# Kernel optimization log

Measured on AMD Instinct MI355X. Metric: run time of the kernel, lower is better.

## Reference

```python
import jax, jax.numpy as jnp
import numpy as np

N_NODES = 100000
N_EDGES = 800000
IN_DIM = 7
HID = 64
HEADS1 = 4
NUM_CLUSTERS = 4
NEG_SLOPE = 0.2


def setup_inputs() -> dict:
    key = jax.random.key(0)
    ks = jax.random.split(key, 24)
    s = 0.1
    inp = {
        "x": jax.random.uniform(ks[0], (N_NODES, IN_DIM), dtype=jnp.float32),
        "edge_index": jax.random.randint(ks[1], (2, N_EDGES), 0, N_NODES, dtype=jnp.int32),
        "edge_attr": jax.random.normal(ks[2], (N_EDGES, 1), dtype=jnp.float32),
        "assignments": jax.random.randint(ks[3], (N_NODES,), 0, NUM_CLUSTERS, dtype=jnp.int32),
        "W1": jax.random.normal(ks[4], (IN_DIM, HEADS1 * HID), dtype=jnp.float32) * s,
        "att_src1": jax.random.normal(ks[5], (HEADS1, HID), dtype=jnp.float32) * s,
        "att_dst1": jax.random.normal(ks[6], (HEADS1, HID), dtype=jnp.float32) * s,
        "We1": jax.random.normal(ks[7], (1, HEADS1 * HID), dtype=jnp.float32) * s,
        "att_e1": jax.random.normal(ks[8], (HEADS1, HID), dtype=jnp.float32) * s,
        "b1": jnp.zeros((HEADS1 * HID,), dtype=jnp.float32),
        "W2": jax.random.normal(ks[9], (HEADS1 * HID, HID), dtype=jnp.float32) * s,
        "att_src2": jax.random.normal(ks[10], (1, HID), dtype=jnp.float32) * s,
        "att_dst2": jax.random.normal(ks[11], (1, HID), dtype=jnp.float32) * s,
        "We2": jax.random.normal(ks[12], (1, HID), dtype=jnp.float32) * s,
        "att_e2": jax.random.normal(ks[13], (1, HID), dtype=jnp.float32) * s,
        "b2": jnp.zeros((HID,), dtype=jnp.float32),
        # actor MLP: (HID+1) -> HID -> 1
        "A1": jax.random.normal(ks[14], (HID + 1, HID), dtype=jnp.float32) * s,
        "ba1": jnp.zeros((HID,), dtype=jnp.float32),
        "A2": jax.random.normal(ks[15], (HID, 1), dtype=jnp.float32) * s,
        "ba2": jnp.zeros((1,), dtype=jnp.float32),
        # critic MLP: HID*num_clusters -> HID -> 1
        "C1": jax.random.normal(ks[16], (HID * NUM_CLUSTERS, HID), dtype=jnp.float32) * s,
        "bc1": jnp.zeros((HID,), dtype=jnp.float32),
        "C2": jax.random.normal(ks[17], (HID, 1), dtype=jnp.float32) * s,
        "bc2": jnp.zeros((1,), dtype=jnp.float32),
    }
    return inp


def _segment_softmax(logits, seg, n):
    # logits: [E, H]; softmax over edges sharing the same dst node.
    m = jax.ops.segment_max(logits, seg, num_segments=n)
    e = jnp.exp(logits - m[seg])
    z = jax.ops.segment_sum(e, seg, num_segments=n)
    return e / z[seg]


def _gat_conv(x, edge_index, edge_attr, W, att_src, att_dst, We, att_e, bias,
              heads, out_dim, concat, n):
    src, dst = edge_index[0], edge_index[1]
    xh = (x @ W).reshape(n, heads, out_dim)                   # [N,H,D]
    a_src = (xh * att_src[None]).sum(-1)                      # [N,H]
    a_dst = (xh * att_dst[None]).sum(-1)                      # [N,H]
    eh = (edge_attr @ We).reshape(-1, heads, out_dim)         # [E,H,D]
    a_e = (eh * att_e[None]).sum(-1)                          # [E,H]
    alpha = jax.nn.leaky_relu(a_src[src] + a_dst[dst] + a_e, NEG_SLOPE)
    alpha = _segment_softmax(alpha, dst, n)                   # [E,H]
    msg = xh[src] * alpha[:, :, None]                         # [E,H,D]
    out = jax.ops.segment_sum(msg, dst, num_segments=n)       # [N,H,D]
    out = out.reshape(n, heads * out_dim) if concat else out.mean(axis=1)
    return out + bias


def reference(x, edge_index, edge_attr, assignments,
              W1, att_src1, att_dst1, We1, att_e1, b1,
              W2, att_src2, att_dst2, We2, att_e2, b2,
              A1, ba1, A2, ba2, C1, bc1, C2, bc2):
    n = x.shape[0]
    h = jax.nn.elu(_gat_conv(x, edge_index, edge_attr,
                             W1, att_src1, att_dst1, We1, att_e1, b1,
                             HEADS1, HID, True, n))
    h = _gat_conv(h, edge_index, edge_attr,
                  W2, att_src2, att_dst2, We2, att_e2, b2,
                  1, HID, False, n)                            # [N,HID]
    # cluster mean pooling (fused segment-reduce, replaces python loop)
    seg = assignments
    counts = jax.ops.segment_sum(jnp.ones((n,), dtype=h.dtype), seg,
                                 num_segments=NUM_CLUSTERS)
    denom = jnp.maximum(counts, 1.0)[:, None]
    z_clusters = jax.ops.segment_sum(h, seg, num_segments=NUM_CLUSTERS) / denom
    z_clusters = jnp.where(counts[:, None] > 0, z_clusters, 0.0)  # [C,HID]
    cf = jax.ops.segment_sum(x[:, 6], seg, num_segments=NUM_CLUSTERS) / denom[:, 0]
    cf = jnp.where(counts > 0, cf, 0.0)[:, None]                  # [C,1]
    z_with_cf = jnp.concatenate([z_clusters, cf], axis=-1)        # [C,HID+1]
    logits = (jax.nn.relu(z_with_cf @ A1 + ba1) @ A2 + ba2)[:, 0]  # [C]
    z_flat = z_clusters.reshape(1, -1)                             # [1,C*HID]
    value = jax.nn.relu(z_flat @ C1 + bc1) @ C2 + bc2              # [1,1]
    probs = jax.nn.softmax(logits)[None, :]                        # [1,C]
    return probs, value, z_flat
```

## Files before the change

### kernel.cpp

```cpp
#include <hip/hip_runtime.h>
#include <hip/hip_fp16.h>

#define NN 100000
#define NE 800000
#define NZB (NN / 32)
#define SRCMASK 0x01FFFFFF

typedef short bf16x8 __attribute__((ext_vector_type(8)));
typedef float f32x4 __attribute__((ext_vector_type(4)));

__device__ __forceinline__ float wave_reduce_sum(float v) {
    #pragma unroll
    for (int o = 32; o > 0; o >>= 1) v += __shfl_down(v, o, 64);
    return v;
}

__device__ __forceinline__ unsigned short f2bf(float f) {
    unsigned u = __float_as_uint(f);
    unsigned r = (u + 0x7FFFu + ((u >> 16) & 1u)) >> 16;
    return (unsigned short)r;
}
__device__ __forceinline__ float bf2f(unsigned short b) {
    return __uint_as_float(((unsigned)b) << 16);
}
__device__ __forceinline__ float bflo(unsigned u) {
    return __uint_as_float(u << 16);
}
__device__ __forceinline__ float bfhi(unsigned u) {
    return __uint_as_float(u & 0xFFFF0000u);
}
__device__ __forceinline__ unsigned pk2(float a, float b) {
    return (unsigned)f2bf(a) | ((unsigned)f2bf(b) << 16);
}
__device__ __forceinline__ unsigned char f2fp8(float f) {
    __half h = __float2half(f * 0.00390625f);
    unsigned short b = __half_as_ushort(h);
    unsigned s = (b >> 8) & 0x80u;
    unsigned mag = b & 0x7FFFu;
    mag = (mag + 0x3Fu + ((mag >> 7) & 1u)) >> 7;
    if (mag > 0x7Eu) mag = 0x7Eu;
    return (unsigned char)(s | mag);
}
__device__ __forceinline__ float dfp8(unsigned v) {
    unsigned short hb = (unsigned short)(((v & 0x80u) << 8) | ((v & 0x7Fu) << 7));
    return __half2float(__ushort_as_half(hb)) * 256.f;
}

__global__ void k_pre(const float* __restrict__ W1, const float* __restrict__ as1,
                      const float* __restrict__ ad1,
                      const float* __restrict__ We1, const float* __restrict__ ae1,
                      const float* __restrict__ We2, const float* __restrict__ ae2,
                      const float* __restrict__ W2, const float* __restrict__ as2,
                      const float* __restrict__ ad2,
                      float* __restrict__ cb, unsigned short* __restrict__ W2fr) {
    int t = threadIdx.x;
    if (blockIdx.x == 0) {
        if (t < 28) {
            int k = t >> 2, h = t & 3;
            float s = 0.f, d = 0.f;
            for (int c = 0; c < 64; ++c) {
                float w = W1[k * 256 + h * 64 + c];
                s += w * as1[h * 64 + c];
                d += w * ad1[h * 64 + c];
            }
            cb[t] = s; cb[28 + t] = d;
        } else if (t < 32) {
            int h = t - 28;
            float s = 0.f;
            for (int c = 0; c < 64; ++c) s += We1[h * 64 + c] * ae1[h * 64 + c];
            cb[56 + h] = s;
        } else if (t == 32) {
            float s = 0.f;
            for (int c = 0; c < 64; ++c) s += We2[c] * ae2[c];
            cb[60] = s;
        }
    } else {
        int o = (blockIdx.x - 1) * 256 + t;
        if (o >= 20480) return;
        int i = o & 7, l = (o >> 3) & 63, rest = o >> 9;
        int ct = rest % 5, ks = rest / 5;
        int k = ks * 32 + ((l >> 4) * 8) + i;
        int cl = l & 15;
        if (ct < 4) {
            W2fr[o] = f2bf(W2[k * 64 + ct * 16 + cl]);
        } else if (cl < 2) {
            const float* av = (cl == 0) ? as2 : ad2;
            float s = 0.f;
            for (int j = 0; j < 64; ++j) s += W2[k * 64 + j] * av[j];
            W2fr[o] = f2bf(s);
        } else {
            W2fr[o] = 0;
        }
    }
}

__global__ void k_node1h(const float* __restrict__ x, const float* __restrict__ cb,
                         const int* __restrict__ dst,
                         uint4* __restrict__ anode, uint4* __restrict__ xpack,
                         int* __restrict__ hist, int* __restrict__ rank) {
    int n = blockIdx.x * 256 + threadIdx.x;
    if (n >= NN) return;
    float xv[7];
    #pragma unroll
    for (int k = 0; k < 7; ++k) xv[k] = x[n * 7 + k];
    float s[4] = {0.f, 0.f, 0.f, 0.f}, d[4] = {0.f, 0.f, 0.f, 0.f};
    #pragma unroll
    for (int k = 0; k < 7; ++k)
        #pragma unroll
        for (int h = 0; h < 4; ++h) {
            s[h] += xv[k] * cb[k * 4 + h];
            d[h] += xv[k] * cb[28 + k * 4 + h];
        }
    anode[n] = make_uint4(pk2(s[0], s[1]), pk2(s[2], s[3]), pk2(d[0], d[1]), pk2(d[2], d[3]));
    xpack[n] = make_uint4(pk2(xv[0], xv[1]), pk2(xv[2], xv[3]),
                          pk2(xv[4], xv[5]), pk2(xv[6], 1.f));
    int e0 = n * 8;
    int4 d0 = *(const int4*)(dst + e0);
    int4 d1 = *(const int4*)(dst + e0 + 4);
    int4 r0, r1;
    r0.x = atomicAdd(&hist[d0.x], 1); r0.y = atomicAdd(&hist[d0.y], 1);
    r0.z = atomicAdd(&hist[d0.z], 1); r0.w = atomicAdd(&hist[d0.w], 1);
    r1.x = atomicAdd(&hist[d1.x], 1); r1.y = atomicAdd(&hist[d1.y], 1);
    r1.z = atomicAdd(&hist[d1.z], 1); r1.w = atomicAdd(&hist[d1.w], 1);
    *(int4*)(rank + e0) = r0;
    *(int4*)(rank + e0 + 4) = r1;
}

__global__ __launch_bounds__(1024) void k_scanA(const int* __restrict__ hist,
                                                int* __restrict__ bsum) {
    __shared__ int ws[16];
    int i = blockIdx.x * 1024 + threadIdx.x;
    int lane = threadIdx.x & 63, wid = threadIdx.x >> 6;
    int v = (i < NN) ? hist[i] : 0;
    #pragma unroll
    for (int o = 32; o; o >>= 1) v += __shfl_down(v, o, 64);
    if (lane == 0) ws[wid] = v;
    __syncthreads();
    if (wid == 0) {
        int u = (lane < 16) ? ws[lane] : 0;
        #pragma unroll
        for (int o = 8; o; o >>= 1) u += __shfl_down(u, o, 64);
        if (lane == 0) bsum[blockIdx.x] = u;
    }
}

__global__ void k_scanB(const int* __restrict__ bsum, int* __restrict__ bexcl) {
    __shared__ int w0tot;
    int t = threadIdx.x, lane = t & 63, wid = t >> 6;
    int v = (t < 98) ? bsum[t] : 0;
    int s = v;
    #pragma unroll
    for (int d = 1; d < 64; d <<= 1) { int u = __shfl_up(s, d, 64); if (lane >= d) s += u; }
    if (t == 63) w0tot = s;
    __syncthreads();
    if (wid == 1) s += w0tot;
    if (t < 98) bexcl[t] = s - v;
}

__global__ __launch_bounds__(1024) void k_scanC(const int* __restrict__ hist,
                                                const int* __restrict__ bexcl,
                                                int* __restrict__ offs) {
    __shared__ int ws[16];
    int b = blockIdx.x;
    int i = b * 1024 + threadIdx.x;
    int lane = threadIdx.x & 63, wid = threadIdx.x >> 6;
    int v = (i < NN) ? hist[i] : 0;
    int s = v;
    #pragma unroll
    for (int d = 1; d < 64; d <<= 1) { int u = __shfl_up(s, d, 64); if (lane >= d) s += u; }
    if (lane == 63) ws[wid] = s;
    __syncthreads();
    if (wid == 0) {
        int u2 = (lane < 16) ? ws[lane] : 0;
        #pragma unroll
        for (int d = 1; d < 16; d <<= 1) { int uu = __shfl_up(u2, d, 64); if (lane >= d) u2 += uu; }
        if (lane < 16) ws[lane] = u2;
    }
    __syncthreads();
    int incl = s + (wid ? ws[wid - 1] : 0) + bexcl[b];
    if (i < NN) offs[i + 1] = incl;
    if (i == 0) offs[0] = 0;
}

__global__ void k_scatter(const int* __restrict__ src, const int* __restrict__ dst,
                          const float* __restrict__ ea, const int* __restrict__ rank,
                          const int* __restrict__ offs,
                          const uint4* __restrict__ anode, const float* __restrict__ cb,
                          int4* __restrict__ es2) {
    int e0 = (blockIdx.x * 256 + threadIdx.x) * 2;
    if (e0 >= NE) return;
    int2 s2 = *(const int2*)(src + e0);
    int2 d2 = *(const int2*)(dst + e0);
    float2 a2 = *(const float2*)(ea + e0);
    int2 r2 = *(const int2*)(rank + e0);
    float c56 = cb[56], c57 = cb[57], c58 = cb[58], c59 = cb[59];
    #pragma unroll
    for (int u = 0; u < 2; ++u) {
        int s = u ? s2.y : s2.x;
        int d = u ? d2.y : d2.x;
        float eav = u ? a2.y : a2.x;
        int pos = offs[d] + (u ? r2.y : r2.x);
        uint4 ar = anode[s];
        uint4 br = anode[d];
        float lg0 = bflo(ar.x) + bflo(br.z) + eav * c56;
        float lg1 = bfhi(ar.x) + bfhi(br.z) + eav * c57;
        float lg2 = bflo(ar.y) + bflo(br.w) + eav * c58;
        float lg3 = bfhi(ar.y) + bfhi(br.w) + eav * c59;
        lg0 = lg0 >= 0.f ? lg0 : 0.2f * lg0;
        lg1 = lg1 >= 0.f ? lg1 : 0.2f * lg1;
        lg2 = lg2 >= 0.f ? lg2 : 0.2f * lg2;
        lg3 = lg3 >= 0.f ? lg3 : 0.2f * lg3;
        unsigned w01 = pk2(__expf(lg0), __expf(lg1));
        unsigned w23 = pk2(__expf(lg2), __expf(lg3));
        es2[pos] = make_int4((int)w01, (int)w23, s | ((d & 31) << 25), __float_as_int(eav));
    }
}

__global__ __launch_bounds__(256, 7) void k_conv1red(
    const uint4* __restrict__ xpack, const float* __restrict__ W1, const float* __restrict__ b1,
    const int* __restrict__ offs, const int4* __restrict__ es2,
    const unsigned short* __restrict__ W2fr,
    unsigned char* __restrict__ xh2f, float* __restrict__ a_src2, float* __restrict__ a_dst2) {
    __shared__ __attribute__((aligned(16))) unsigned char smem[16896];
    uint4* xs = (uint4*)smem;
    uint2* wsx = (uint2*)(smem + 4096);
    typedef unsigned short hsrow[264];
    hsrow* hs = (hsrow*)smem;
    __shared__ int soffs[33];
    __shared__ float ms[32][33];
    int t = threadIdx.x, lane = t & 63, wid = t >> 6;
    int n0 = blockIdx.x * 32;
    if (t <= 32) soffs[t] = offs[n0 + t];
    float w1r[7][4], b1r[4];
    #pragma unroll
    for (int k = 0; k < 7; ++k)
        #pragma unroll
        for (int h = 0; h < 4; ++h) w1r[k][h] = W1[k * 256 + h * 64 + lane];
    #pragma unroll
    for (int h = 0; h < 4; ++h) b1r[h] = b1[h * 64 + lane];
    __syncthreads();
    int E0 = soffs[0], E1 = soffs[32];
    int g = t >> 3, q = t & 7;
    int go0 = soffs[g], go1 = soffs[g + 1];
    int qh = q >> 1;
    int xsl = (q & 1) ? 0 : 16;
    float mh0 = 0.f, mh1 = 0.f, mh2 = 0.f, mh3 = 0.f;
    for (int C0 = E0; C0 < E1; C0 += 256) {
        int C1 = min(C0 + 256, E1);
        int j = C0 + t;
        if (j < C1) {
            int4 e4 = es2[j];
            xs[t] = xpack[e4.z & SRCMASK];
            wsx[t] = make_uint2((unsigned)e4.x, (unsigned)e4.y);
        }
        __syncthreads();
        int lo = max(go0, C0) - C0, hi = min(go1, C1) - C0;
        for (int jj = lo; jj < hi; ++jj) {
            unsigned xu = ((const unsigned*)&xs[jj])[qh];
            float xv = __uint_as_float((xu << xsl) & 0xFFFF0000u);
            uint2 wv = wsx[jj];
            mh0 = fmaf(bflo(wv.x), xv, mh0);
            mh1 = fmaf(bfhi(wv.x), xv, mh1);
            mh2 = fmaf(bflo(wv.y), xv, mh2);
            mh3 = fmaf(bfhi(wv.y), xv, mh3);
        }
        __syncthreads();
    }
    ms[g][0 * 8 + q] = mh0; ms[g][1 * 8 + q] = mh1;
    ms[g][2 * 8 + q] = mh2; ms[g][3 * 8 + q] = mh3;
    __syncthreads();
    for (int gi = wid * 8; gi < wid * 8 + 8; ++gi) {
        bool has = soffs[gi + 1] > soffs[gi];
        #pragma unroll
        for (int h = 0; h < 4; ++h) {
            float rz = __builtin_amdgcn_rcpf(ms[gi][h * 8 + 7]);
            float a = 0.f;
            #pragma unroll
            for (int k = 0; k < 7; ++k) a = fmaf(ms[gi][h * 8 + k], w1r[k][h], a);
            float mm = (has ? a * rz : 0.f) + b1r[h];
            float hv = mm > 0.f ? mm : (__expf(mm) - 1.f);
            hs[gi][h * 64 + lane] = f2bf(hv);
        }
    }
    __syncthreads();
    int row = lane & 15, kg = lane >> 4;
    #pragma unroll
    for (int u = wid; u < 10; u += 4) {
        int nt = u & 1, ct = u >> 1;
        f32x4 acc = {0.f, 0.f, 0.f, 0.f};
        #pragma unroll
        for (int ks = 0; ks < 8; ++ks) {
            bf16x8 av = *(const bf16x8*)&hs[nt * 16 + row][ks * 32 + kg * 8];
            bf16x8 bv = *(const bf16x8*)(W2fr + (((ks * 5 + ct) * 64) + lane) * 8);
            acc = __builtin_amdgcn_mfma_f32_16x16x32_bf16(av, bv, acc, 0, 0, 0);
        }
        if (ct < 4) {
            #pragma unroll
            for (int i = 0; i < 4; ++i)
                xh2f[(n0 + nt * 16 + kg * 4 + i) * 64 + ct * 16 + row] = f2fp8(acc[i]);
        } else if (row == 0) {
            #pragma unroll
            for (int i = 0; i < 4; ++i) a_src2[n0 + nt * 16 + kg * 4 + i] = acc[i];
        } else if (row == 1) {
            #pragma unroll
            for (int i = 0; i < 4; ++i) a_dst2[n0 + nt * 16 + kg * 4 + i] = acc[i];
        }
    }
}

__global__ __launch_bounds__(256) void k_zpool(
    const int4* __restrict__ es2, const int* __restrict__ offs,
    const float* __restrict__ a_src2, const float* __restrict__ a_dst2,
    const int* __restrict__ assign, const float* __restrict__ cb,
    const unsigned char* __restrict__ xh2f, const float* __restrict__ x,
    float* __restrict__ partial) {
    __shared__ int soffs[33];
    __shared__ float adL[32];
    __shared__ int asgL[32];
    __shared__ float ewL[512];
    __shared__ int sL[512];
    __shared__ float rzL[32];
    __shared__ float zacc[32];
    __shared__ float csum[264];
    int t = threadIdx.x;
    int n0 = blockIdx.x * 32;
    if (t <= 32) soffs[t] = offs[n0 + t];
    if (t < 32) { adL[t] = a_dst2[n0 + t]; asgL[t] = assign[n0 + t]; zacc[t] = 0.f; }
    for (int i = t; i < 264; i += 256) csum[i] = 0.f;
    __syncthreads();
    int E0 = soffs[0], E1 = soffs[32];
    float c2 = cb[60];
    if (E0 + t < E1) {
        int4 e4 = es2[E0 + t];
        int sx = e4.z & SRCMASK;
        int d5 = (e4.z >> 25) & 31;
        float lg = a_src2[sx] + adL[d5] + __int_as_float(e4.w) * c2;
        lg = lg >= 0.f ? lg : 0.2f * lg;
        ewL[t] = __expf(lg);
        sL[t] = sx;
    }
    if (E0 + 256 + t < E1) {
        int4 e4 = es2[E0 + 256 + t];
        int sx = e4.z & SRCMASK;
        int d5 = (e4.z >> 25) & 31;
        float lg = a_src2[sx] + adL[d5] + __int_as_float(e4.w) * c2;
        lg = lg >= 0.f ? lg : 0.2f * lg;
        ewL[256 + t] = __expf(lg);
        sL[256 + t] = sx;
    }
    for (int j = E0 + 512 + t; j < E1; j += 256) {
        int4 e4 = es2[j];
        int d5 = (e4.z >> 25) & 31;
        float lg = a_src2[e4.z & SRCMASK] + adL[d5] + __int_as_float(e4.w) * c2;
        lg = lg >= 0.f ? lg : 0.2f * lg;
        atomicAdd(&zacc[d5], __expf(lg));
    }
    __syncthreads();
    int g = t >> 3, q = t & 7;
    int lo = soffs[g] - E0, hi = soffs[g + 1] - E0;
    int hicap = min(hi, 512);
    float z = 0.f;
    for (int jj = lo + q; jj < hicap; jj += 8) z += ewL[jj];
    z += __shfl_xor(z, 1, 64);
    z += __shfl_xor(z, 2, 64);
    z += __shfl_xor(z, 4, 64);
    if (q == 0) rzL[g] = __builtin_amdgcn_rcpf(z + zacc[g]);
    __syncthreads();
    float rzv = rzL[g];
    float a0 = 0.f, a1 = 0.f, a2 = 0.f, a3 = 0.f;
    float a4 = 0.f, a5 = 0.f, a6 = 0.f, a7 = 0.f;
    for (int jj = lo; jj < hicap; ++jj) {
        float wv = ewL[jj] * rzv;
        int sj = sL[jj];
        uint2 u = *(const uint2*)(xh2f + sj * 64 + q * 8);
        a0 = fmaf(wv, dfp8(u.x & 255u), a0);
        a1 = fmaf(wv, dfp8((u.x >> 8) & 255u), a1);
        a2 = fmaf(wv, dfp8((u.x >> 16) & 255u), a2);
        a3 = fmaf(wv, dfp8(u.x >> 24), a3);
        a4 = fmaf(wv, dfp8(u.y & 255u), a4);
        a5 = fmaf(wv, dfp8((u.y >> 8) & 255u), a5);
        a6 = fmaf(wv, dfp8((u.y >> 16) & 255u), a6);
        a7 = fmaf(wv, dfp8(u.y >> 24), a7);
    }
    for (int jo = max(lo, 512); jo < hi; ++jo) {
        int4 e4 = es2[E0 + jo];
        int sx = e4.z & SRCMASK;
        float lg = a_src2[sx] + adL[g] + __int_as_float(e4.w) * c2;
        lg = lg >= 0.f ? lg : 0.2f * lg;
        float wv = __expf(lg) * rzv;
        uint2 u = *(const uint2*)(xh2f + sx * 64 + q * 8);
        a0 = fmaf(wv, dfp8(u.x & 255u), a0);
        a1 = fmaf(wv, dfp8((u.x >> 8) & 255u), a1);
        a2 = fmaf(wv, dfp8((u.x >> 16) & 255u), a2);
        a3 = fmaf(wv, dfp8(u.x >> 24), a3);
        a4 = fmaf(wv, dfp8(u.y & 255u), a4);
        a5 = fmaf(wv, dfp8((u.y >> 8) & 255u), a5);
        a6 = fmaf(wv, dfp8((u.y >> 16) & 255u), a6);
        a7 = fmaf(wv, dfp8(u.y >> 24), a7);
    }
    int cb_ = asgL[g] * 64 + q * 8;
    atomicAdd(&csum[cb_ + 0], a0); atomicAdd(&csum[cb_ + 1], a1);
    atomicAdd(&csum[cb_ + 2], a2); atomicAdd(&csum[cb_ + 3], a3);
    atomicAdd(&csum[cb_ + 4], a4); atomicAdd(&csum[cb_ + 5], a5);
    atomicAdd(&csum[cb_ + 6], a6); atomicAdd(&csum[cb_ + 7], a7);
    if (t < 32) {
        int c = asgL[t];
        atomicAdd(&csum[256 + c], 1.f);
        atomicAdd(&csum[260 + c], x[(n0 + t) * 7 + 6]);
    }
    __syncthreads();
    for (int i = t; i < 264; i += 256) partial[blockIdx.x * 264 + i] = csum[i];
}

__global__ void k_red(const float* __restrict__ partial, float* __restrict__ gacc) {
    int i = blockIdx.x;
    float s = 0.f;
    for (int b = threadIdx.x; b < NZB; b += 64) s += partial[b * 264 + i];
    s = wave_reduce_sum(s);
    if (threadIdx.x == 0) gacc[i] = s;
}

__global__ __launch_bounds__(256) void k_head(
    const float* __restrict__ gacc, const float* __restrict__ b2,
    const float* __restrict__ A1, const float* __restrict__ ba1,
    const float* __restrict__ A2, const float* __restrict__ ba2,
    const float* __restrict__ C1, const float* __restrict__ bc1,
    const float* __restrict__ C2, const float* __restrict__ bc2,
    float* __restrict__ out) {
    __shared__ float zc[4][64];
    __shared__ float cfs[4];
    __shared__ float logits[4];
    __shared__ float vpart[4][64];
    int t = threadIdx.x;
    int j = t & 63, wv = t >> 6;
    float cnt = gacc[256 + wv];
    float den = fmaxf(cnt, 1.f);
    zc[wv][j] = (cnt > 0.f) ? (gacc[wv * 64 + j] + cnt * b2[j]) / den : 0.f;
    if (t < 4) {
        float cc = gacc[256 + t];
        cfs[t] = (cc > 0.f) ? gacc[260 + t] / fmaxf(cc, 1.f) : 0.f;
    }
    __syncthreads();
    float tv = ba1[j];
    for (int k = 0; k < 64; ++k) tv = fmaf(zc[wv][k], A1[k * 64 + j], tv);
    tv = fmaf(cfs[wv], A1[64 * 64 + j], tv);
    tv = fmaxf(tv, 0.f);
    float sred = wave_reduce_sum(tv * A2[j]);
    if (j == 0) logits[wv] = sred + ba2[0];
    float vj = (wv == 0) ? bc1[j] : 0.f;
    for (int kk = 0; kk < 64; ++kk) vj = fmaf(zc[wv][kk], C1[(wv * 64 + kk) * 64 + j], vj);
    vpart[wv][j] = vj;
    __syncthreads();
    if (wv == 0) {
        float vv = fmaxf(vpart[0][j] + vpart[1][j] + vpart[2][j] + vpart[3][j], 0.f);
        float v = wave_reduce_sum(vv * C2[j]);
        if (j == 0) {
            float m = fmaxf(fmaxf(logits[0], logits[1]), fmaxf(logits[2], logits[3]));
            float e0 = __expf(logits[0] - m), e1 = __expf(logits[1] - m);
            float e2 = __expf(logits[2] - m), e3 = __expf(logits[3] - m);
            float sum = e0 + e1 + e2 + e3;
            out[0] = e0 / sum; out[1] = e1 / sum; out[2] = e2 / sum; out[3] = e3 / sum;
            out[4] = v + bc2[0];
        }
    }
    out[5 + wv * 64 + j] = zc[wv][j];
}

extern "C" void kernel_launch(void* const* d_in, const int* in_sizes, int n_in,
                              void* d_out, int out_size, void* d_ws, size_t ws_size,
                              hipStream_t stream) {
    const float* x    = (const float*)d_in[0];
    const int*   ei   = (const int*)d_in[1];
    const float* ea   = (const float*)d_in[2];
    const int*   asg  = (const int*)d_in[3];
    const float* W1   = (const float*)d_in[4];
    const float* as1  = (const float*)d_in[5];
    const float* ad1  = (const float*)d_in[6];
    const float* We1  = (const float*)d_in[7];
    const float* ae1  = (const float*)d_in[8];
    const float* b1   = (const float*)d_in[9];
    const float* W2   = (const float*)d_in[10];
    const float* as2  = (const float*)d_in[11];
    const float* ad2  = (const float*)d_in[12];
    const float* We2  = (const float*)d_in[13];
    const float* ae2  = (const float*)d_in[14];
    const float* b2   = (const float*)d_in[15];
    const float* A1   = (const float*)d_in[16];
    const float* ba1  = (const float*)d_in[17];
    const float* A2   = (const float*)d_in[18];
    const float* ba2  = (const float*)d_in[19];
    const float* C1   = (const float*)d_in[20];
    const float* bc1  = (const float*)d_in[21];
    const float* C2   = (const float*)d_in[22];
    const float* bc2  = (const float*)d_in[23];
    const int* src = ei;
    const int* dst = ei + NE;

    char* w = (char*)d_ws;
    size_t off = 0;
    auto alloc = [&](size_t bytes) -> void* {
        void* p = w + off;
        off += (bytes + 255) & ~(size_t)255;
        return p;
    };
    int*   hist   = (int*)alloc(NN * sizeof(int));
    float* gacc   = (float*)alloc(264 * sizeof(float));
    float* partial= (float*)alloc((size_t)NZB * 264 * sizeof(float));
    uint4* anode  = (uint4*)alloc(NN * sizeof(uint4));
    float* a_src2 = (float*)alloc(NN * sizeof(float));
    float* a_dst2 = (float*)alloc(NN * sizeof(float));
    uint4* xpack  = (uint4*)alloc(NN * sizeof(uint4));
    int*   offs   = (int*)alloc((NN + 1) * sizeof(int));
    int*   rank   = (int*)alloc(NE * sizeof(int));
    int*   bsum   = (int*)alloc(128 * sizeof(int));
    int*   bexcl  = (int*)alloc(128 * sizeof(int));
    int4*  es2    = (int4*)alloc(NE * sizeof(int4));
    unsigned char* xh2f = (unsigned char*)alloc(NN * 64 * sizeof(unsigned char));
    unsigned short* W2fr = (unsigned short*)alloc(20480 * sizeof(unsigned short));
    float* cb     = (float*)alloc(64 * sizeof(float));
    (void)ws_size; (void)n_in; (void)in_sizes; (void)out_size;

    (void)hipMemsetAsync(hist, 0, NN * sizeof(int), stream);

    k_pre<<<81, 256, 0, stream>>>(W1, as1, ad1, We1, ae1, We2, ae2, W2, as2, ad2, cb, W2fr);
    k_node1h<<<(NN + 255) / 256, 256, 0, stream>>>(x, cb, dst, anode, xpack, hist, rank);
    k_scanA<<<98, 1024, 0, stream>>>(hist, bsum);
    k_scanB<<<1, 128, 0, stream>>>(bsum, bexcl);
    k_scanC<<<98, 1024, 0, stream>>>(hist, bexcl, offs);
    k_scatter<<<(NE / 2 + 255) / 256, 256, 0, stream>>>(src, dst, ea, rank, offs,
                                                        anode, cb, es2);
    k_conv1red<<<NN / 32, 256, 0, stream>>>(xpack, W1, b1, offs, es2,
                                            W2fr, xh2f, a_src2, a_dst2);
    k_zpool<<<NZB, 256, 0, stream>>>(es2, offs, a_src2, a_dst2, asg, cb, xh2f, x, partial);
    k_red<<<264, 64, 0, stream>>>(partial, gacc);
    k_head<<<1, 256, 0, stream>>>(gacc, b2, A1, ba1, A2, ba2, C1, bc1, C2, bc2, (float*)d_out);
}
```

Measured before the change: 186.3 us.

## Balance zpool aggregation by striding edges across groups with per-cluster accumulators

The weighted aggregation in k_zpool now distributes all of a block's edges evenly across the 32 thread groups instead of giving each group one destination node's edges, removing load imbalance from degree variance. Each thread keeps 4x8 per-cluster accumulators, selected by the destination's cluster assignment, and reduces them with wave shuffles before shared-memory atomics. The edge list now stores the packed src/dst word so the destination and its normaliser can be recovered per edge. This costs four times more FMAs per edge and higher register pressure in exchange for balanced work.

```diff
diff --git a/kernel.cpp b/kernel.cpp
--- a/kernel.cpp
+++ b/kernel.cpp
@@ -329,27 +329,28 @@
     for (int i = t; i < 264; i += 256) csum[i] = 0.f;
     __syncthreads();
     int E0 = soffs[0], E1 = soffs[32];
+    int span = E1 - E0;
     float c2 = cb[60];
-    if (E0 + t < E1) {
+    if (t < span) {
         int4 e4 = es2[E0 + t];
         int sx = e4.z & SRCMASK;
         int d5 = (e4.z >> 25) & 31;
         float lg = a_src2[sx] + adL[d5] + __int_as_float(e4.w) * c2;
         lg = lg >= 0.f ? lg : 0.2f * lg;
         ewL[t] = __expf(lg);
-        sL[t] = sx;
-    }
-    if (E0 + 256 + t < E1) {
+        sL[t] = e4.z;
+    }
+    if (256 + t < span) {
         int4 e4 = es2[E0 + 256 + t];
         int sx = e4.z & SRCMASK;
         int d5 = (e4.z >> 25) & 31;
         float lg = a_src2[sx] + adL[d5] + __int_as_float(e4.w) * c2;
         lg = lg >= 0.f ? lg : 0.2f * lg;
         ewL[256 + t] = __expf(lg);
-        sL[256 + t] = sx;
-    }
-    for (int j = E0 + 512 + t; j < E1; j += 256) {
-        int4 e4 = es2[j];
+        sL[256 + t] = e4.z;
+    }
+    for (int j = 512 + t; j < span; j += 256) {
+        int4 e4 = es2[E0 + j];
         int d5 = (e4.z >> 25) & 31;
         float lg = a_src2[e4.z & SRCMASK] + adL[d5] + __int_as_float(e4.w) * c2;
         lg = lg >= 0.f ? lg : 0.2f * lg;
@@ -366,43 +367,66 @@
     z += __shfl_xor(z, 4, 64);
     if (q == 0) rzL[g] = __builtin_amdgcn_rcpf(z + zacc[g]);
     __syncthreads();
-    float rzv = rzL[g];
-    float a0 = 0.f, a1 = 0.f, a2 = 0.f, a3 = 0.f;
-    float a4 = 0.f, a5 = 0.f, a6 = 0.f, a7 = 0.f;
-    for (int jj = lo; jj < hicap; ++jj) {
-        float wv = ewL[jj] * rzv;
-        int sj = sL[jj];
-        uint2 u = *(const uint2*)(xh2f + sj * 64 + q * 8);
-        a0 = fmaf(wv, dfp8(u.x & 255u), a0);
-        a1 = fmaf(wv, dfp8((u.x >> 8) & 255u), a1);
-        a2 = fmaf(wv, dfp8((u.x >> 16) & 255u), a2);
-        a3 = fmaf(wv, dfp8(u.x >> 24), a3);
-        a4 = fmaf(wv, dfp8(u.y & 255u), a4);
-        a5 = fmaf(wv, dfp8((u.y >> 8) & 255u), a5);
-        a6 = fmaf(wv, dfp8((u.y >> 16) & 255u), a6);
-        a7 = fmaf(wv, dfp8(u.y >> 24), a7);
-    }
-    for (int jo = max(lo, 512); jo < hi; ++jo) {
-        int4 e4 = es2[E0 + jo];
-        int sx = e4.z & SRCMASK;
-        float lg = a_src2[sx] + adL[g] + __int_as_float(e4.w) * c2;
-        lg = lg >= 0.f ? lg : 0.2f * lg;
-        float wv = __expf(lg) * rzv;
-        uint2 u = *(const uint2*)(xh2f + sx * 64 + q * 8);
-        a0 = fmaf(wv, dfp8(u.x & 255u), a0);
-        a1 = fmaf(wv, dfp8((u.x >> 8) & 255u), a1);
-        a2 = fmaf(wv, dfp8((u.x >> 16) & 255u), a2);
-        a3 = fmaf(wv, dfp8(u.x >> 24), a3);
-        a4 = fmaf(wv, dfp8(u.y & 255u), a4);
-        a5 = fmaf(wv, dfp8((u.y >> 8) & 255u), a5);
-        a6 = fmaf(wv, dfp8((u.y >> 16) & 255u), a6);
-        a7 = fmaf(wv, dfp8(u.y >> 24), a7);
-    }
-    int cb_ = asgL[g] * 64 + q * 8;
-    atomicAdd(&csum[cb_ + 0], a0); atomicAdd(&csum[cb_ + 1], a1);
-    atomicAdd(&csum[cb_ + 2], a2); atomicAdd(&csum[cb_ + 3], a3);
-    atomicAdd(&csum[cb_ + 4], a4); atomicAdd(&csum[cb_ + 5], a5);
-    atomicAdd(&csum[cb_ + 6], a6); atomicAdd(&csum[cb_ + 7], a7);
+    int slot = t >> 3;
+    const unsigned char* pbase = xh2f + q * 8;
+    float ac[4][8];
+    #pragma unroll
+    for (int c = 0; c < 4; ++c)
+        #pragma unroll
+        for (int k = 0; k < 8; ++k) ac[c][k] = 0.f;
+    #pragma unroll 2
+    for (int jj = slot; jj < span; jj += 32) {
+        int zv; float ew;
+        if (jj < 512) {
+            zv = sL[jj];
+            ew = ewL[jj];
+        } else {
+            int4 e4 = es2[E0 + jj];
+            zv = e4.z;
+            int d5o = (zv >> 25) & 31;
+            float lg = a_src2[zv & SRCMASK] + adL[d5o] + __int_as_float(e4.w) * c2;
+            lg = lg >= 0.f ? lg : 0.2f * lg;
+            ew = __expf(lg);
+        }
+        int sx = zv & SRCMASK;
+        int d5 = (zv >> 25) & 31;
+        float wv = ew * rzL[d5];
+        int cc = asgL[d5];
+        uint2 u = *(const uint2*)(pbase + sx * 64);
+        float v0 = dfp8(u.x & 255u), v1 = dfp8((u.x >> 8) & 255u);
+        float v2 = dfp8((u.x >> 16) & 255u), v3 = dfp8(u.x >> 24);
+        float v4 = dfp8(u.y & 255u), v5 = dfp8((u.y >> 8) & 255u);
+        float v6 = dfp8((u.y >> 16) & 255u), v7 = dfp8(u.y >> 24);
+        #pragma unroll
+        for (int c = 0; c < 4; ++c) {
+            float wc = (cc == c) ? wv : 0.f;
+            ac[c][0] = fmaf(wc, v0, ac[c][0]);
+            ac[c][1] = fmaf(wc, v1, ac[c][1]);
+            ac[c][2] = fmaf(wc, v2, ac[c][2]);
+            ac[c][3] = fmaf(wc, v3, ac[c][3]);
+            ac[c][4] = fmaf(wc, v4, ac[c][4]);
+            ac[c][5] = fmaf(wc, v5, ac[c][5]);
+            ac[c][6] = fmaf(wc, v6, ac[c][6]);
+            ac[c][7] = fmaf(wc, v7, ac[c][7]);
+        }
+    }
+    #pragma unroll
+    for (int c = 0; c < 4; ++c)
+        #pragma unroll
+        for (int k = 0; k < 8; ++k) {
+            float v = ac[c][k];
+            v += __shfl_xor(v, 8, 64);
+            v += __shfl_xor(v, 16, 64);
+            v += __shfl_xor(v, 32, 64);
+            ac[c][k] = v;
+        }
+    if (((t >> 3) & 7) == 0) {
+        #pragma unroll
+        for (int c = 0; c < 4; ++c)
+            #pragma unroll
+            for (int k = 0; k < 8; ++k)
+                atomicAdd(&csum[c * 64 + q * 8 + k], ac[c][k]);
+    }
     if (t < 32) {
         int c = asgL[t];
         atomicAdd(&csum[256 + c], 1.f);
@@ -515,7 +539,7 @@
     int*   bsum   = (int*)alloc(128 * sizeof(int));
     int*   bexcl  = (int*)alloc(128 * sizeof(int));
     int4*  es2    = (int4*)alloc(NE * sizeof(int4));
-    unsigned char* xh2f = (unsigned char*)alloc(NN * 64 * sizeof(unsigned char));
+    unsigned char* xh2f = (unsigned char*)alloc((size_t)NN * 64 * sizeof(unsigned char));
     unsigned short* W2fr = (unsigned short*)alloc(20480 * sizeof(unsigned short));
     float* cb     = (float*)alloc(64 * sizeof(float));
     (void)ws_size; (void)n_in; (void)in_sizes; (void)out_size;
```

Result: faster. 176.9 us (-5.1%).
